# Kernel optimization log

Hardware: AMD Instinct MI355X
Metric: run time of the kernel (lower is better)

## Reference

```python
import jax, jax.numpy as jnp
import numpy as np

H = 2048      # hidden_size
NH = 16       # num_attention_heads
NKV = 4       # num_key_value_heads
HD = 128      # head_dim (= v_head_dim)
RD = 64       # rope_dim = head_dim * partial_rotary_factor
E = 16        # n_routed_experts
G = 4         # n_group
TG = 2        # topk_group
TK = 4        # num_experts_per_tok
FF = 512      # moe_intermediate_size
ROUTE_SCALE = 2.5
EPS = 1e-6


def _rmsnorm(x, w):
    var = jnp.mean(x * x, axis=-1, keepdims=True)
    return w * (x * jax.lax.rsqrt(var + EPS))


def _rotate_half(x):
    x1, x2 = x[..., : x.shape[-1] // 2], x[..., x.shape[-1] // 2:]
    return jnp.concatenate([-x2, x1], axis=-1)


def setup_inputs() -> dict:
    key = jax.random.key(0)
    ks = jax.random.split(key, 12)
    B, S = 1, 2048
    x = jax.random.normal(ks[0], (B, S, H), jnp.float32)
    # partial RoPE tables (rope_dim = 64)
    pos = jnp.arange(S, dtype=jnp.float32)
    inv_freq = 1.0 / (10000.0 ** (jnp.arange(0, RD // 2, dtype=jnp.float32) / (RD // 2)))
    ang = pos[:, None] * inv_freq[None, :]
    emb = jnp.concatenate([ang, ang], axis=-1)  # [S, RD]
    cos, sin = jnp.cos(emb)[None], jnp.sin(emb)[None]  # [1, S, RD]

    def w(k, shape):
        return jax.random.normal(k, shape, jnp.float32) * 0.02

    return dict(
        hidden_states=x, cos=cos, sin=sin,
        ln1_w=jnp.ones((H,), jnp.float32), ln2_w=jnp.ones((H,), jnp.float32),
        Wq=w(ks[1], (H, NH * HD)), Wk=w(ks[2], (H, NKV * HD)),
        Wv=w(ks[3], (H, NKV * HD)), Wo=w(ks[4], (NH * HD, H)),
        sink_bias=w(ks[5], (NH,)),
        gate_w=w(ks[6], (E, H)), gate_bias=w(ks[7], (E,)),
        Weg=w(ks[8], (E, H, FF)), Weu=w(ks[9], (E, H, FF)), Wed=w(ks[10], (E, FF, H)),
    )


def reference(hidden_states, cos, sin, ln1_w, ln2_w, Wq, Wk, Wv, Wo,
              sink_bias, gate_w, gate_bias, Weg, Weu, Wed):
    b, s, _ = hidden_states.shape

    # ---- self-attention (sink-bias softmax, partial RoPE, GQA) ----
    xn = _rmsnorm(hidden_states, ln1_w)
    q = (xn @ Wq).reshape(b, s, NH, HD).transpose(0, 2, 1, 3)    # [b,NH,s,HD]
    k = (xn @ Wk).reshape(b, s, NKV, HD).transpose(0, 2, 1, 3)   # [b,NKV,s,HD]
    v = (xn @ Wv).reshape(b, s, NKV, HD).transpose(0, 2, 1, 3)
    c, sn = cos[:, None], sin[:, None]                           # [b,1,s,RD]
    qr, qn = q[..., :RD], q[..., RD:]
    kr, kn = k[..., :RD], k[..., RD:]
    qr = qr * c + _rotate_half(qr) * sn
    kr = kr * c + _rotate_half(kr) * sn
    q = jnp.concatenate([qr, qn], axis=-1)
    k = jnp.concatenate([kr, kn], axis=-1)
    rep = NH // NKV
    k = jnp.repeat(k, rep, axis=1)
    v = jnp.repeat(v, rep, axis=1)
    scores = jnp.einsum('bhqd,bhkd->bhqk', q, k) * (HD ** -0.5)
    causal = jnp.triu(jnp.ones((s, s), bool), 1)
    scores = jnp.where(causal[None, None], -jnp.inf, scores)
    m = jnp.max(scores, axis=-1, keepdims=True)
    sink_exp = jnp.exp(sink_bias.reshape(1, NH, 1, 1) - m)       # [b,NH,s,1]
    attn_exp = jnp.exp(scores - m)
    probs = attn_exp / (jnp.sum(attn_exp, axis=-1, keepdims=True) + sink_exp)
    ao = jnp.einsum('bhqk,bhkd->bhqd', probs, v)
    attn_out = ao.transpose(0, 2, 1, 3).reshape(b, s, NH * HD) @ Wo
    h1 = hidden_states + attn_out

    # ---- MoE with group-limited top-k gate ----
    xf = _rmsnorm(h1, ln2_w).reshape(-1, H)                      # [n,H]
    n = xf.shape[0]
    logits = xf @ gate_w.T                                       # [n,E]
    scores_g = jax.nn.sigmoid(logits)
    sfc = scores_g + gate_bias[None]
    group_scores = jnp.sum(jax.lax.top_k(sfc.reshape(n, G, E // G), 2)[0], axis=-1)
    gidx = jax.lax.top_k(group_scores, TG)[1]                    # [n,TG]
    gmask = jnp.sum(jax.nn.one_hot(gidx, G, dtype=jnp.float32), axis=1) > 0
    smask = jnp.repeat(gmask, E // G, axis=1)                    # [n,E]
    tmp = jnp.where(smask, sfc, -jnp.inf)
    _, tidx = jax.lax.top_k(tmp, TK)                             # [n,TK]
    tw = jnp.take_along_axis(scores_g, tidx, axis=1)
    tw = tw / (jnp.sum(tw, axis=-1, keepdims=True) + 1e-20)      # norm_topk_prob
    tw = tw * ROUTE_SCALE
    # combine weights: zero for unselected experts (faithful to sparse dispatch)
    cw = jnp.sum(jax.nn.one_hot(tidx, E, dtype=tw.dtype) * tw[..., None], axis=1)  # [n,E]
    g = jnp.einsum('nh,ehf->enf', xf, Weg)
    u = jnp.einsum('nh,ehf->enf', xf, Weu)
    hgu = (jax.nn.silu(g) * u) * cw.T[:, :, None]                # weight before down-proj
    moe_out = jnp.einsum('enf,efh->nh', hgu, Wed)
    return h1 + moe_out.reshape(hidden_states.shape)
```

## Files before the change

### kernel.cpp

```cpp
#include <hip/hip_runtime.h>
#include <math.h>

typedef unsigned short u16;
typedef __bf16 bf16x8 __attribute__((ext_vector_type(8)));
typedef float f32x4 __attribute__((ext_vector_type(4)));

#define SEQ 2048
#define ATT_SCALE 0.08838834764831845f

__device__ __forceinline__ u16 f2bf(float f){
  union{float f;unsigned u;}v; v.f=f;
  unsigned r=v.u + 0x7fffu + ((v.u>>16)&1u);
  return (u16)(r>>16);
}
__device__ __forceinline__ float bf2f(u16 u){
  union{unsigned u;float f;}v; v.u=((unsigned)u)<<16; return v.f;
}
__device__ __forceinline__ f32x4 f4zero(){ f32x4 v; v[0]=0.f;v[1]=0.f;v[2]=0.f;v[3]=0.f; return v; }
__device__ __forceinline__ f32x4 mfma16(bf16x8 a, bf16x8 b, f32x4 c){
  return __builtin_amdgcn_mfma_f32_16x16x32_bf16(a,b,c,0,0,0);
}

typedef const __attribute__((address_space(1))) unsigned char* gas1p;
typedef __attribute__((address_space(3))) unsigned char* las3p;
__device__ __forceinline__ void gld16(const void* g, void* l){
  __builtin_amdgcn_global_load_lds((gas1p)g, (las3p)l, 16, 0, 0);
}

__global__ __launch_bounds__(256) void transpose_cvt_k(const float* __restrict__ in,
                                                       u16* __restrict__ out,
                                                       int R, int C,
                                                       size_t in_stride, size_t out_stride){
  const float* src = in + (size_t)blockIdx.z*in_stride;
  u16* dst = out + (size_t)blockIdx.z*out_stride;
  int tc = blockIdx.x*64;
  int tr = blockIdx.y*64;
  __shared__ float tile[64][65];
  int t=threadIdx.x;
  int lr=t>>4, lc=(t&15)*4;
  #pragma unroll
  for(int i=0;i<4;i++){
    float4 v=*(const float4*)&src[(size_t)(tr+lr+i*16)*C + tc+lc];
    tile[lr+i*16][lc+0]=v.x; tile[lr+i*16][lc+1]=v.y;
    tile[lr+i*16][lc+2]=v.z; tile[lr+i*16][lc+3]=v.w;
  }
  __syncthreads();
  int on=t>>2, kq=(t&3)*16;
  alignas(16) u16 ov[16];
  #pragma unroll
  for(int j=0;j<16;j++) ov[j]=f2bf(tile[kq+j][on]);
  *(uint4*)&dst[(size_t)(tc+on)*R + tr+kq]   = *(uint4*)&ov[0];
  *(uint4*)&dst[(size_t)(tc+on)*R + tr+kq+8] = *(uint4*)&ov[8];
}

__global__ __launch_bounds__(256) void transpose_v_k(const float* __restrict__ qkvf,
                                                     u16* __restrict__ vbT){
  int st=blockIdx.x*64, dt=blockIdx.y*64, kvh=blockIdx.z;
  __shared__ float tile[64][68];
  int t=threadIdx.x;
  #pragma unroll
  for(int i=0;i<4;i++){
    int f=i*256+t; int sr=f>>4, c4=(f&15)*4;
    float4 v=*(const float4*)&qkvf[(size_t)(st+sr)*3072 + 2560 + kvh*128 + dt + c4];
    tile[sr][c4]=v.x; tile[sr][c4+1]=v.y; tile[sr][c4+2]=v.z; tile[sr][c4+3]=v.w;
  }
  __syncthreads();
  #pragma unroll
  for(int i=0;i<2;i++){
    int f=i*256+t; int dr=f>>3, sc=(f&7)*8;
    alignas(16) u16 ov[8];
    #pragma unroll
    for(int j=0;j<8;j++) ov[j]=f2bf(tile[sc+j][dr]);
    *(uint4*)&vbT[((size_t)kvh*128 + dt+dr)*2048 + st + sc]=*(uint4*)ov;
  }
}

__global__ __launch_bounds__(256) void rmsnorm_k(const float* __restrict__ x,
                                                 const float* __restrict__ w,
                                                 u16* __restrict__ o){
  int row=blockIdx.x, t=threadIdx.x;
  const float* xr = x + (size_t)row*2048;
  float4 a=*(const float4*)&xr[t*8], b=*(const float4*)&xr[t*8+4];
  float ss = a.x*a.x+a.y*a.y+a.z*a.z+a.w*a.w + b.x*b.x+b.y*b.y+b.z*b.z+b.w*b.w;
  #pragma unroll
  for(int m=1;m<=32;m<<=1) ss += __shfl_xor(ss,m);
  __shared__ float red[4];
  if((t&63)==0) red[t>>6]=ss;
  __syncthreads();
  float tot = red[0]+red[1]+red[2]+red[3];
  float inv = rsqrtf(tot*(1.0f/2048.0f)+1e-6f);
  const float* wr = w + t*8;
  float4 wa=*(const float4*)&wr[0], wb=*(const float4*)&wr[4];
  alignas(16) u16 ov[8];
  ov[0]=f2bf(a.x*inv*wa.x); ov[1]=f2bf(a.y*inv*wa.y);
  ov[2]=f2bf(a.z*inv*wa.z); ov[3]=f2bf(a.w*inv*wa.w);
  ov[4]=f2bf(b.x*inv*wb.x); ov[5]=f2bf(b.y*inv*wb.y);
  ov[6]=f2bf(b.z*inv*wb.z); ov[7]=f2bf(b.w*inv*wb.w);
  *(uint4*)&o[(size_t)row*2048 + t*8] = *(uint4*)ov;
}

template<int MODE>
__global__ __launch_bounds__(256) void gemm_bt_k(const u16* __restrict__ A,
                                                 const u16* __restrict__ BT0,
                                                 const u16* __restrict__ BT1,
                                                 float* __restrict__ Cf,
                                                 u16* __restrict__ Cb,
                                                 const float* __restrict__ hid,
                                                 const int* __restrict__ counts,
                                                 const int* __restrict__ offsets,
                                                 const int* __restrict__ toklist,
                                                 int K, int ldc, int NMT, int NBY){
  __shared__ alignas(16) u16 Al[2][64*64];
  __shared__ alignas(16) u16 Bl[2][128*64];
  __shared__ int slist[64];
  int t=threadIdx.x, lane=t&63, wid=t>>6;
  int nwg=gridDim.x, q=nwg>>3;
  int l=(blockIdx.x&7)*q + (blockIdx.x>>3);
  int e=0, mt, by;
  if constexpr(MODE>=2){
    int per=NMT*NBY;
    e=l/per; int rem=l-e*per;
    mt=(rem%NMT)*64; by=rem/NMT;
  } else {
    mt=(l%NMT)*64; by=l/NMT;
  }
  int cnt=0, off=0;
  if constexpr(MODE>=2){
    cnt=counts[e]; off=offsets[e];
    if(mt>=cnt) return;
  }
  const u16* Bbase;
  int cb=by*128;
  if constexpr(MODE==2){
    if(by<4) Bbase = BT0 + ((size_t)e*512 + by*128)*(size_t)K;
    else     Bbase = BT1 + ((size_t)e*512 + (by-4)*128)*(size_t)K;
  } else if constexpr(MODE==3){
    Bbase = BT0 + ((size_t)e*2048 + (size_t)cb)*(size_t)K;
  } else {
    Bbase = BT0 + (size_t)cb*(size_t)K;
  }
  if constexpr(MODE==2){
    if(t<64){
      int gr=mt+t; if(gr>=cnt) gr=cnt-1;
      slist[t]=toklist[off+gr];
    }
    __syncthreads();
  }
  int srow=t>>3;
  int sc=((t&7)^(srow&7))*8;
  const u16* aptr[2]; const u16* bptr[4];
  #pragma unroll
  for(int i=0;i<2;i++){
    int r=i*32+srow;
    size_t arow;
    if constexpr(MODE==2) arow=(size_t)slist[r];
    else if constexpr(MODE==3){ int s=off+mt+r; if(s>8191)s=8191; arow=(size_t)s; }
    else arow=(size_t)(mt+r);
    aptr[i]=A + arow*(size_t)K + sc;
  }
  #pragma unroll
  for(int i=0;i<4;i++){
    int r=i*32+srow;
    bptr[i]=Bbase + (size_t)r*(size_t)K + sc;
  }
  int fm=lane&15, fo=lane>>4;
  int wm=(wid>>1)*32, wn=(wid&1)*64;
  int aoff[2][2], boff[4][2];
  #pragma unroll
  for(int m=0;m<2;m++){
    int row=wm+m*16+fm;
    #pragma unroll
    for(int kk=0;kk<2;kk++) aoff[m][kk]=row*64 + (((kk*4+fo)^(row&7))*8);
  }
  #pragma unroll
  for(int n=0;n<4;n++){
    int row=wn+n*16+fm;
    #pragma unroll
    for(int kk=0;kk<2;kk++) boff[n][kk]=row*64 + (((kk*4+fo)^(row&7))*8);
  }
  f32x4 acc[2][4];
  #pragma unroll
  for(int m=0;m<2;m++)
    #pragma unroll
    for(int n=0;n<4;n++) acc[m][n]=f4zero();
  int ntk=K>>6;
  #pragma unroll
  for(int i=0;i<2;i++) gld16(aptr[i], &Al[0][i*2048+wid*512]);
  #pragma unroll
  for(int i=0;i<4;i++) gld16(bptr[i], &Bl[0][i*2048+wid*512]);
  __syncthreads();
  for(int kt=0;kt<ntk;kt++){
    int cur=kt&1;
    if(kt+1<ntk){
      int k0=(kt+1)<<6, nb=cur^1;
      #pragma unroll
      for(int i=0;i<2;i++) gld16(aptr[i]+k0, &Al[nb][i*2048+wid*512]);
      #pragma unroll
      for(int i=0;i<4;i++) gld16(bptr[i]+k0, &Bl[nb][i*2048+wid*512]);
    }
    bf16x8 af[2][2], bv[4][2];
    #pragma unroll
    for(int m=0;m<2;m++){
      af[m][0]=*(const bf16x8*)&Al[cur][aoff[m][0]];
      af[m][1]=*(const bf16x8*)&Al[cur][aoff[m][1]];
    }
    #pragma unroll
    for(int n=0;n<4;n++){
      bv[n][0]=*(const bf16x8*)&Bl[cur][boff[n][0]];
      bv[n][1]=*(const bf16x8*)&Bl[cur][boff[n][1]];
    }
    #pragma unroll
    for(int m=0;m<2;m++)
      #pragma unroll
      for(int n=0;n<4;n++){
        acc[m][n]=mfma16(af[m][0],bv[n][0],acc[m][n]);
        acc[m][n]=mfma16(af[m][1],bv[n][1],acc[m][n]);
      }
    __syncthreads();
  }
  #pragma unroll
  for(int m=0;m<2;m++)
    #pragma unroll
    for(int n=0;n<4;n++)
      #pragma unroll
      for(int r=0;r<4;r++){
        int lr=wm+m*16+fo*4+r;
        int col=cb+wn+n*16+fm;
        float v=acc[m][n][r];
        if constexpr(MODE==0){
          Cf[(size_t)(mt+lr)*ldc+col]=v;
        } else if constexpr(MODE==1){
          size_t idx=(size_t)(mt+lr)*ldc+col;
          Cf[idx]=v+hid[idx];
        } else if constexpr(MODE==2){
          int gr=mt+lr;
          if(gr<cnt) Cb[(size_t)(off+gr)*1024+col]=f2bf(v);
        } else {
          int gr=mt+lr;
          if(gr<cnt) Cb[(size_t)(off+gr)*2048+col]=f2bf(v);
        }
      }
}

__global__ __launch_bounds__(256) void moe_reduce_k(const u16* __restrict__ moeb,
                                                    const int* __restrict__ slotof,
                                                    float* __restrict__ out){
  int n=blockIdx.x, t=threadIdx.x;
  int4 s4=*(const int4*)&slotof[n*4];
  int c=t*8;
  const u16* r0=moeb+(size_t)s4.x*2048+c;
  const u16* r1=moeb+(size_t)s4.y*2048+c;
  const u16* r2=moeb+(size_t)s4.z*2048+c;
  const u16* r3=moeb+(size_t)s4.w*2048+c;
  uint4 a=*(const uint4*)r0, b=*(const uint4*)r1,
        cc=*(const uint4*)r2, d=*(const uint4*)r3;
  const u16* pa=(const u16*)&a; const u16* pb=(const u16*)&b;
  const u16* pc=(const u16*)&cc; const u16* pd=(const u16*)&d;
  float* op=out+(size_t)n*2048+c;
  float4 o0=*(const float4*)op, o1=*(const float4*)(op+4);
  float ov[8]={o0.x,o0.y,o0.z,o0.w,o1.x,o1.y,o1.z,o1.w};
  #pragma unroll
  for(int j=0;j<8;j++)
    ov[j]+=bf2f(pa[j])+bf2f(pb[j])+bf2f(pc[j])+bf2f(pd[j]);
  *(float4*)op    =make_float4(ov[0],ov[1],ov[2],ov[3]);
  *(float4*)(op+4)=make_float4(ov[4],ov[5],ov[6],ov[7]);
}

__global__ __launch_bounds__(256) void rope_pack_k(const float* __restrict__ qkvf,
                                                   const float* __restrict__ cosb,
                                                   const float* __restrict__ sinb,
                                                   u16* __restrict__ qb,
                                                   u16* __restrict__ kb){
  int s=blockIdx.x, t=threadIdx.x;
  __shared__ float cs[64], sn[64];
  if(t<64){ cs[t]=cosb[s*64+t]; sn[t]=sinb[s*64+t]; }
  __syncthreads();
  {
    int idx=t*8; int d=idx&127;
    const float* src=qkvf+(size_t)s*3072+idx;
    float4 a=*(const float4*)src, b=*(const float4*)(src+4);
    float v[8]={a.x,a.y,a.z,a.w,b.x,b.y,b.z,b.w};
    alignas(16) u16 o[8];
    if(d<64){
      const float* ps=(d<32)? src+32 : src-32;
      float4 pa=*(const float4*)ps, pb=*(const float4*)(ps+4);
      float p[8]={pa.x,pa.y,pa.z,pa.w,pb.x,pb.y,pb.z,pb.w};
      #pragma unroll
      for(int j=0;j<8;j++){
        float c=cs[d+j], si=sn[d+j];
        float r=(d<32)? (v[j]*c - p[j]*si) : (v[j]*c + p[j]*si);
        o[j]=f2bf(r);
      }
    } else {
      #pragma unroll
      for(int j=0;j<8;j++) o[j]=f2bf(v[j]);
    }
    *(uint4*)&qb[(size_t)s*2048+idx]=*(uint4*)o;
  }
  if(t<64){
    int idx=t*8; int kvh=idx>>7; int d=idx&127;
    const float* src=qkvf+(size_t)s*3072+2048+idx;
    float4 a=*(const float4*)src, b=*(const float4*)(src+4);
    float v[8]={a.x,a.y,a.z,a.w,b.x,b.y,b.z,b.w};
    alignas(16) u16 o[8];
    if(d<64){
      const float* ps=(d<32)? src+32 : src-32;
      float4 pa=*(const float4*)ps, pb=*(const float4*)(ps+4);
      float p[8]={pa.x,pa.y,pa.z,pa.w,pb.x,pb.y,pb.z,pb.w};
      #pragma unroll
      for(int j=0;j<8;j++){
        float c=cs[d+j], si=sn[d+j];
        float r=(d<32)? (v[j]*c - p[j]*si) : (v[j]*c + p[j]*si);
        o[j]=f2bf(r);
      }
    } else {
      #pragma unroll
      for(int j=0;j<8;j++) o[j]=f2bf(v[j]);
    }
    *(uint4*)&kb[((size_t)kvh*SEQ + s)*128 + d]=*(uint4*)o;
  }
}

__global__ __launch_bounds__(256) void attn_k(const u16* __restrict__ qb,
                                              const u16* __restrict__ kb,
                                              const u16* __restrict__ vbT,
                                              const float* __restrict__ sink,
                                              u16* __restrict__ ao){
  int h=blockIdx.x;
  int qt=31-blockIdx.y;
  int kvh=h>>2;
  int t=threadIdx.x, wid=t>>6, lane=t&63;
  int fm=lane&15, fo=lane>>4;
  int qbase=qt*64;
  __shared__ alignas(16) u16 Kl[2][64*128];
  __shared__ alignas(16) u16 Vl[2][128*64];
  __shared__ alignas(16) u16 Pl[4][16*72];
  bf16x8 qfr[4];
  int qrow=qbase+wid*16+fm;
  #pragma unroll
  for(int c=0;c<4;c++)
    qfr[c]=*(const bf16x8*)&qb[(size_t)qrow*2048 + h*128 + c*32 + fo*8];
  f32x4 o[8];
  #pragma unroll
  for(int dg=0;dg<8;dg++) o[dg]=f4zero();
  float mr[4]={-1e30f,-1e30f,-1e30f,-1e30f};
  float ls[4]={0.f,0.f,0.f,0.f};
  const u16* kbase=kb+(size_t)kvh*SEQ*128;
  const u16* vtb=vbT+(size_t)kvh*128*SEQ;
  int nt=qt+1;
  u16* pw=&Pl[wid][0];
  {
    #pragma unroll
    for(int i=0;i<4;i++){
      int fc=(wid*4+i)*64+lane;
      int row=fc>>4, g=(fc&15)^(row&15);
      gld16(kbase+(size_t)row*128+g*8, &Kl[0][(wid*4+i)*512]);
    }
    #pragma unroll
    for(int i=0;i<4;i++){
      int fc=(wid*4+i)*64+lane;
      int row=fc>>3, g=(fc&7)^(row&7);
      gld16(vtb+(size_t)row*2048+g*8, &Vl[0][(wid*4+i)*512]);
    }
  }
  __syncthreads();
  for(int tt=0;tt<nt;tt++){
    int cur=tt&1;
    if(tt+1<nt){
      int kv0n=(tt+1)*64, nb=cur^1;
      #pragma unroll
      for(int i=0;i<4;i++){
        int fc=(wid*4+i)*64+lane;
        int row=fc>>4, g=(fc&15)^(row&15);
        gld16(kbase+(size_t)(kv0n+row)*128+g*8, &Kl[nb][(wid*4+i)*512]);
      }
      #pragma unroll
      for(int i=0;i<4;i++){
        int fc=(wid*4+i)*64+lane;
        int row=fc>>3, g=(fc&7)^(row&7);
        gld16(vtb+(size_t)row*2048+kv0n+g*8, &Vl[nb][(wid*4+i)*512]);
      }
    }
    int kv0=tt*64;
    f32x4 s[4];
    #pragma unroll
    for(int ss=0;ss<4;ss++) s[ss]=f4zero();
    #pragma unroll
    for(int c=0;c<4;c++){
      #pragma unroll
      for(int ss=0;ss<4;ss++){
        int row=ss*16+fm;
        bf16x8 kf=*(const bf16x8*)&Kl[cur][row*128 + (((c*4+fo)^(row&15))*8)];
        s[ss]=mfma16(qfr[c],kf,s[ss]);
      }
    }
    bool diag=(tt==nt-1);
    int qg=qbase+wid*16+fo*4;
    #pragma unroll
    for(int r=0;r<4;r++){
      float v0=s[0][r]*ATT_SCALE, v1=s[1][r]*ATT_SCALE,
            v2=s[2][r]*ATT_SCALE, v3=s[3][r]*ATT_SCALE;
      if(diag){
        int qr=qg+r;
        if(kv0+   fm > qr) v0=-1e30f;
        if(kv0+16+fm > qr) v1=-1e30f;
        if(kv0+32+fm > qr) v2=-1e30f;
        if(kv0+48+fm > qr) v3=-1e30f;
      }
      float vm=fmaxf(fmaxf(v0,v1),fmaxf(v2,v3));
      vm=fmaxf(vm,__shfl_xor(vm,1)); vm=fmaxf(vm,__shfl_xor(vm,2));
      vm=fmaxf(vm,__shfl_xor(vm,4)); vm=fmaxf(vm,__shfl_xor(vm,8));
      float mn=fmaxf(mr[r],vm);
      float sc=__expf(mr[r]-mn);
      mr[r]=mn;
      float p0=__expf(v0-mn), p1=__expf(v1-mn),
            p2=__expf(v2-mn), p3=__expf(v3-mn);
      float rs=(p0+p1)+(p2+p3);
      rs+=__shfl_xor(rs,1); rs+=__shfl_xor(rs,2);
      rs+=__shfl_xor(rs,4); rs+=__shfl_xor(rs,8);
      ls[r]=ls[r]*sc+rs;
      #pragma unroll
      for(int dg=0;dg<8;dg++) o[dg][r]*=sc;
      int prow=(fo*4+r)*72;
      pw[prow+fm   ]=f2bf(p0);
      pw[prow+16+fm]=f2bf(p1);
      pw[prow+32+fm]=f2bf(p2);
      pw[prow+48+fm]=f2bf(p3);
    }
    #pragma unroll
    for(int kvs=0;kvs<2;kvs++){
      bf16x8 pa=*(const bf16x8*)&pw[fm*72 + kvs*32 + fo*8];
      #pragma unroll
      for(int dg=0;dg<8;dg++){
        int R=dg*16+fm;
        bf16x8 bv=*(const bf16x8*)&Vl[cur][R*64 + (((kvs*4+fo)^(R&7))*8)];
        o[dg]=mfma16(pa,bv,o[dg]);
      }
    }
    __syncthreads();
  }
  float sb=sink[h];
  float invd[4];
  #pragma unroll
  for(int r=0;r<4;r++) invd[r]=1.f/(ls[r]+__expf(sb-mr[r]));
  #pragma unroll
  for(int dg=0;dg<8;dg++)
    #pragma unroll
    for(int r=0;r<4;r++){
      int row=qbase+wid*16+fo*4+r;
      ao[(size_t)row*2048 + h*128 + dg*16 + fm]=f2bf(o[dg][r]*invd[r]);
    }
}

__global__ __launch_bounds__(256) void gate_route_k(const float* __restrict__ h1,
                                                    const float* __restrict__ lnw,
                                                    const float* __restrict__ gw,
                                                    const float* __restrict__ gb,
                                                    int* __restrict__ tsel,
                                                    float* __restrict__ twsel){
  int n=blockIdx.x, t=threadIdx.x, lane=t&63, wid=t>>6;
  const float* xr=h1+(size_t)n*2048;
  float4 a=*(const float4*)&xr[t*8], b=*(const float4*)&xr[t*8+4];
  float xv[8]={a.x,a.y,a.z,a.w,b.x,b.y,b.z,b.w};
  float ss=0.f;
  #pragma unroll
  for(int j=0;j<8;j++) ss+=xv[j]*xv[j];
  #pragma unroll
  for(int m=1;m<=32;m<<=1) ss+=__shfl_xor(ss,m);
  __shared__ float redn[4];
  if(lane==0) redn[wid]=ss;
  __syncthreads();
  float inv=rsqrtf((redn[0]+redn[1]+redn[2]+redn[3])*(1.0f/2048.0f)+1e-6f);
  const float* wr=lnw+t*8;
  float4 wa=*(const float4*)&wr[0], wb=*(const float4*)&wr[4];
  float wv[8]={wa.x,wa.y,wa.z,wa.w,wb.x,wb.y,wb.z,wb.w};
  #pragma unroll
  for(int j=0;j<8;j++) xv[j]*=inv*wv[j];
  float part[16];
  #pragma unroll
  for(int e=0;e<16;e++){
    const float* g=gw+(size_t)e*2048+t*8;
    float4 ga=*(const float4*)&g[0], gb2=*(const float4*)&g[4];
    part[e]=xv[0]*ga.x+xv[1]*ga.y+xv[2]*ga.z+xv[3]*ga.w
           +xv[4]*gb2.x+xv[5]*gb2.y+xv[6]*gb2.z+xv[7]*gb2.w;
  }
  #pragma unroll
  for(int e=0;e<16;e++)
    #pragma unroll
    for(int m=1;m<=32;m<<=1) part[e]+=__shfl_xor(part[e],m);
  __shared__ float red[4][16];
  __shared__ float lg[16];
  if(lane<16) red[wid][lane]=part[lane];
  __syncthreads();
  if(t<16) lg[t]=red[0][t]+red[1][t]+red[2][t]+red[3][t];
  __syncthreads();
  if(t==0){
    float sg[16], sfc[16];
    #pragma unroll
    for(int e=0;e<16;e++){ sg[e]=1.f/(1.f+__expf(-lg[e])); sfc[e]=sg[e]+gb[e]; }
    float gs[4];
    #pragma unroll
    for(int g=0;g<4;g++){
      const float* v=&sfc[g*4];
      int im=0;
      for(int j=1;j<4;j++) if(v[j]>v[im]) im=j;
      float m2=-1e30f;
      for(int j=0;j<4;j++) if(j!=im && v[j]>m2) m2=v[j];
      gs[g]=v[im]+m2;
    }
    int g1=0;
    for(int j=1;j<4;j++) if(gs[j]>gs[g1]) g1=j;
    int g2=-1;
    for(int j=0;j<4;j++){ if(j==g1) continue; if(g2<0||gs[j]>gs[g2]) g2=j; }
    bool used[16];
    for(int e=0;e<16;e++) used[e]=false;
    int ch[4]; float tw[4];
    for(int s=0;s<4;s++){
      int best=-1; float bvv=-1e30f;
      for(int e=0;e<16;e++){
        int g=e>>2;
        if(g!=g1 && g!=g2) continue;
        if(used[e]) continue;
        if(sfc[e]>bvv){ bvv=sfc[e]; best=e; }
      }
      used[best]=true; ch[s]=best; tw[s]=sg[best];
    }
    float ssum=tw[0]+tw[1]+tw[2]+tw[3]+1e-20f;
    float sc=2.5f/ssum;
    for(int s=0;s<4;s++){ tsel[n*4+s]=ch[s]; twsel[n*4+s]=tw[s]*sc; }
  }
}

__global__ __launch_bounds__(256) void scan_fill_k(const int* __restrict__ tsel,
                                                   const float* __restrict__ twsel,
                                                   int* __restrict__ counts,
                                                   int* __restrict__ offsets,
                                                   int* __restrict__ toklist,
                                                   float* __restrict__ wslot,
                                                   int* __restrict__ slotof){
  __shared__ int cnt[16], off[16], cur[16];
  int t=threadIdx.x;
  if(t<16){ cnt[t]=0; cur[t]=0; }
  __syncthreads();
  for(int n=t;n<2048;n+=256)
    for(int j=0;j<4;j++) atomicAdd(&cnt[tsel[n*4+j]],1);
  __syncthreads();
  if(t==0){
    int run=0;
    for(int e=0;e<16;e++){ off[e]=run; run+=cnt[e]; }
  }
  __syncthreads();
  if(t<16){ counts[t]=cnt[t]; offsets[t]=off[t]; }
  for(int n=t;n<2048;n+=256)
    for(int j=0;j<4;j++){
      int e=tsel[n*4+j];
      int pos=atomicAdd(&cur[e],1);
      int slot=off[e]+pos;
      toklist[slot]=n;
      wslot[slot]=twsel[n*4+j];
      slotof[n*4+j]=slot;
    }
}

__global__ __launch_bounds__(256) void hgu_act_k(const u16* __restrict__ gu,
                                                 const float* __restrict__ wslot,
                                                 u16* __restrict__ hgu){
  int t=threadIdx.x;
  int slot=blockIdx.x*4+(t>>6);
  int f8=(t&63)*8;
  float wv=wslot[slot];
  uint4 gr=*(const uint4*)&gu[(size_t)slot*1024+f8];
  uint4 ur=*(const uint4*)&gu[(size_t)slot*1024+512+f8];
  const u16* gp=(const u16*)&gr;
  const u16* up=(const u16*)&ur;
  alignas(16) u16 o[8];
  #pragma unroll
  for(int j=0;j<8;j++){
    float g=bf2f(gp[j]), u=bf2f(up[j]);
    float s=g/(1.f+__expf(-g));
    o[j]=f2bf(s*u*wv);
  }
  *(uint4*)&hgu[(size_t)slot*512+f8]=*(uint4*)o;
}

extern "C" void kernel_launch(void* const* d_in, const int* in_sizes, int n_in,
                              void* d_out, int out_size, void* d_ws, size_t ws_size,
                              hipStream_t stream){
  const float* x    =(const float*)d_in[0];
  const float* cosb =(const float*)d_in[1];
  const float* sinb =(const float*)d_in[2];
  const float* ln1w =(const float*)d_in[3];
  const float* ln2w =(const float*)d_in[4];
  const float* Wq   =(const float*)d_in[5];
  const float* Wk   =(const float*)d_in[6];
  const float* Wv   =(const float*)d_in[7];
  const float* Wo   =(const float*)d_in[8];
  const float* sink =(const float*)d_in[9];
  const float* gw   =(const float*)d_in[10];
  const float* gb   =(const float*)d_in[11];
  const float* Weg  =(const float*)d_in[12];
  const float* Weu  =(const float*)d_in[13];
  const float* Wed  =(const float*)d_in[14];
  float* out=(float*)d_out;
  char* w=(char*)d_ws;
  const size_t MB=1024*1024;
  float* qkvf=(float*)(w+0);
  u16* gu =(u16*)(w+0);
  u16* hgu=(u16*)(w+16*MB);
  u16* xn =(u16*)(w+24*MB);
  u16* qb =(u16*)(w+32*MB);
  u16* kb =(u16*)(w+40*MB);
  u16* vbT=(u16*)(w+42*MB);
  u16* aob=(u16*)(w+44*MB);
  u16* xfb=(u16*)(w+52*MB);
  int*   tsel   =(int*)(w+60*MB);
  float* twsel  =(float*)(w+60*MB+32768);
  int*   counts =(int*)(w+60*MB+65536);
  int*   offsets=(int*)(w+60*MB+65536+256);
  int*   toklist=(int*)(w+60*MB+65536+512);
  float* wslot  =(float*)(w+60*MB+65536+512+32768);
  int*   slotof =(int*)(w+60*MB+65536+512+65536);
  char* wt=w+61*MB;
  u16* WqT=(u16*)(wt);
  u16* WkT=(u16*)(wt+8*MB);
  u16* WvT=(u16*)(wt+10*MB);
  u16* WoT=(u16*)(wt+12*MB);
  u16* WegT=(u16*)(wt);
  u16* WeuT=(u16*)(wt+32*MB);
  u16* WedT=(u16*)(wt);
  u16* moeb=(u16*)(wt+32*MB);

  dim3 blk(256);
  transpose_cvt_k<<<dim3(32,32,1),blk,0,stream>>>(Wq, WqT, 2048,2048, 0,0);
  transpose_cvt_k<<<dim3(8,32,1), blk,0,stream>>>(Wk, WkT, 2048,512, 0,0);
  transpose_cvt_k<<<dim3(8,32,1), blk,0,stream>>>(Wv, WvT, 2048,512, 0,0);
  transpose_cvt_k<<<dim3(32,32,1),blk,0,stream>>>(Wo, WoT, 2048,2048, 0,0);
  rmsnorm_k<<<dim3(2048),blk,0,stream>>>(x, ln1w, xn);
  gemm_bt_k<0><<<dim3(768),blk,0,stream>>>(xn, WqT,nullptr, qkvf,nullptr,nullptr,
                                           nullptr,nullptr,nullptr, 2048,3072, 32,24);
  rope_pack_k<<<dim3(2048),blk,0,stream>>>(qkvf,cosb,sinb,qb,kb);
  transpose_v_k<<<dim3(32,2,4),blk,0,stream>>>(qkvf, vbT);
  attn_k<<<dim3(16,32),blk,0,stream>>>(qb,kb,vbT,sink,aob);
  gemm_bt_k<1><<<dim3(512),blk,0,stream>>>(aob, WoT,nullptr, out,nullptr,x,
                                           nullptr,nullptr,nullptr, 2048,2048, 32,16);
  rmsnorm_k<<<dim3(2048),blk,0,stream>>>(out, ln2w, xfb);
  gate_route_k<<<dim3(2048),blk,0,stream>>>(out, ln2w, gw, gb, tsel, twsel);
  scan_fill_k<<<dim3(1),blk,0,stream>>>(tsel, twsel, counts, offsets, toklist, wslot, slotof);
  transpose_cvt_k<<<dim3(8,32,16),blk,0,stream>>>(Weg, WegT, 2048,512, 1048576,1048576);
  transpose_cvt_k<<<dim3(8,32,16),blk,0,stream>>>(Weu, WeuT, 2048,512, 1048576,1048576);
  gemm_bt_k<2><<<dim3(4096),blk,0,stream>>>(xfb, WegT,WeuT, nullptr,gu,nullptr,
                                            counts,offsets,toklist, 2048,1024, 32,8);
  hgu_act_k<<<dim3(2048),blk,0,stream>>>(gu, wslot, hgu);
  transpose_cvt_k<<<dim3(32,8,16),blk,0,stream>>>(Wed, WedT, 512,2048, 1048576,1048576);
  gemm_bt_k<3><<<dim3(8192),blk,0,stream>>>(hgu, WedT,nullptr, nullptr,moeb,nullptr,
                                            counts,offsets,toklist, 512,2048, 32,16);
  moe_reduce_k<<<dim3(2048),blk,0,stream>>>(moeb, slotof, out);
}
```

Baseline: 390.1 us.

## Read K/V fragments directly from global memory in attention, dropping LDS staging

The attention kernel stops double-buffering K and V tiles in shared memory via async global-to-LDS loads and instead has each wave load its MFMA operand fragments straight from global memory (relying on L1/L2 cache). This removes the per-tile __syncthreads and frees most of the LDS, and the launch bound now requests 4 blocks per CU for higher occupancy. In exchange, each K/V element is loaded from global by all four waves, and loads are no longer prefetched ahead of compute, so latency is exposed unless occupancy hides it.

```diff
diff --git a/kernel.cpp b/kernel.cpp
--- a/kernel.cpp
+++ b/kernel.cpp
@@ -321,19 +321,17 @@
   }
 }
 
-__global__ __launch_bounds__(256) void attn_k(const u16* __restrict__ qb,
-                                              const u16* __restrict__ kb,
-                                              const u16* __restrict__ vbT,
-                                              const float* __restrict__ sink,
-                                              u16* __restrict__ ao){
+__global__ __launch_bounds__(256,4) void attn_k(const u16* __restrict__ qb,
+                                                const u16* __restrict__ kb,
+                                                const u16* __restrict__ vbT,
+                                                const float* __restrict__ sink,
+                                                u16* __restrict__ ao){
   int h=blockIdx.x;
   int qt=31-blockIdx.y;
   int kvh=h>>2;
   int t=threadIdx.x, wid=t>>6, lane=t&63;
   int fm=lane&15, fo=lane>>4;
   int qbase=qt*64;
-  __shared__ alignas(16) u16 Kl[2][64*128];
-  __shared__ alignas(16) u16 Vl[2][128*64];
   __shared__ alignas(16) u16 Pl[4][16*72];
   bf16x8 qfr[4];
   int qrow=qbase+wid*16+fm;
@@ -349,48 +347,17 @@
   const u16* vtb=vbT+(size_t)kvh*128*SEQ;
   int nt=qt+1;
   u16* pw=&Pl[wid][0];
-  {
-    #pragma unroll
-    for(int i=0;i<4;i++){
-      int fc=(wid*4+i)*64+lane;
-      int row=fc>>4, g=(fc&15)^(row&15);
-      gld16(kbase+(size_t)row*128+g*8, &Kl[0][(wid*4+i)*512]);
-    }
-    #pragma unroll
-    for(int i=0;i<4;i++){
-      int fc=(wid*4+i)*64+lane;
-      int row=fc>>3, g=(fc&7)^(row&7);
-      gld16(vtb+(size_t)row*2048+g*8, &Vl[0][(wid*4+i)*512]);
-    }
-  }
-  __syncthreads();
   for(int tt=0;tt<nt;tt++){
-    int cur=tt&1;
-    if(tt+1<nt){
-      int kv0n=(tt+1)*64, nb=cur^1;
-      #pragma unroll
-      for(int i=0;i<4;i++){
-        int fc=(wid*4+i)*64+lane;
-        int row=fc>>4, g=(fc&15)^(row&15);
-        gld16(kbase+(size_t)(kv0n+row)*128+g*8, &Kl[nb][(wid*4+i)*512]);
-      }
-      #pragma unroll
-      for(int i=0;i<4;i++){
-        int fc=(wid*4+i)*64+lane;
-        int row=fc>>3, g=(fc&7)^(row&7);
-        gld16(vtb+(size_t)row*2048+kv0n+g*8, &Vl[nb][(wid*4+i)*512]);
-      }
-    }
     int kv0=tt*64;
     f32x4 s[4];
     #pragma unroll
     for(int ss=0;ss<4;ss++) s[ss]=f4zero();
     #pragma unroll
-    for(int c=0;c<4;c++){
-      #pragma unroll
-      for(int ss=0;ss<4;ss++){
-        int row=ss*16+fm;
-        bf16x8 kf=*(const bf16x8*)&Kl[cur][row*128 + (((c*4+fo)^(row&15))*8)];
+    for(int ss=0;ss<4;ss++){
+      const u16* krow=kbase+(size_t)(kv0+ss*16+fm)*128 + fo*8;
+      #pragma unroll
+      for(int c=0;c<4;c++){
+        bf16x8 kf=*(const bf16x8*)&krow[c*32];
         s[ss]=mfma16(qfr[c],kf,s[ss]);
       }
     }
@@ -432,12 +399,10 @@
       bf16x8 pa=*(const bf16x8*)&pw[fm*72 + kvs*32 + fo*8];
       #pragma unroll
       for(int dg=0;dg<8;dg++){
-        int R=dg*16+fm;
-        bf16x8 bv=*(const bf16x8*)&Vl[cur][R*64 + (((kvs*4+fo)^(R&7))*8)];
+        bf16x8 bv=*(const bf16x8*)&vtb[(size_t)(dg*16+fm)*2048 + kv0 + kvs*32 + fo*8];
         o[dg]=mfma16(pa,bv,o[dg]);
       }
     }
-    __syncthreads();
   }
   float sb=sink[h];
   float invd[4];
```

Measured after the change: 505.3 us. 1.3x slower.
